# Kernel tuning notes

Hardware: AMD Instinct MI355X
Metric: run time of the kernel (lower is better)

The kernel has to match this reference:

```python
import jax, jax.numpy as jnp
import numpy as np
from jax import lax

DIM = 256
HEADS = 8
HIDDEN = int(DIM * 2.66)  # 680
KS = 3


def conv1x1(x, w, b):
    # x: (B,C,H,W), w: (O,C), b: (O,)
    return jnp.einsum('oc,bchw->bohw', w, x) + b[None, :, None, None]


def dwconv(x, w, b):
    # depthwise 3x3, SAME padding; w: (C,1,3,3)
    y = lax.conv_general_dilated(
        x, w, window_strides=(1, 1), padding='SAME',
        feature_group_count=x.shape[1],
        dimension_numbers=('NCHW', 'OIHW', 'NCHW'))
    return y + b[None, :, None, None]


def layernorm_c(x, w, b, eps=1e-5):
    # torch nn.LayerNorm(dim) applied on NHWC -> normalize over channel dim
    mu = jnp.mean(x, axis=1, keepdims=True)
    var = jnp.mean(jnp.square(x - mu), axis=1, keepdims=True)
    xn = (x - mu) * lax.rsqrt(var + eps)
    return xn * w[None, :, None, None] + b[None, :, None, None]


def l2norm(x, eps=1e-12):
    # F.normalize(dim=-1)
    n = jnp.sqrt(jnp.sum(jnp.square(x), axis=-1, keepdims=True))
    return x / jnp.maximum(n, eps)


def setup_inputs() -> dict:
    key = jax.random.key(0)
    ks = jax.random.split(key, 20)
    s = 0.02
    d = {
        'x': jax.random.normal(ks[0], (4, DIM, 128, 128), jnp.float32),
        'n1_w': jnp.ones((DIM,), jnp.float32),
        'n1_b': jnp.zeros((DIM,), jnp.float32),
        'temp': jnp.ones((HEADS, 1, 1), jnp.float32),
        'qkv_w': jax.random.normal(ks[1], (3 * DIM, DIM), jnp.float32) * s,
        'qkv_b': jnp.zeros((3 * DIM,), jnp.float32),
        'qkv_dw_w': jax.random.normal(ks[2], (3 * DIM, 1, KS, KS), jnp.float32) * s,
        'qkv_dw_b': jnp.zeros((3 * DIM,), jnp.float32),
        'attn_po_w': jax.random.normal(ks[3], (DIM, DIM), jnp.float32) * s,
        'attn_po_b': jnp.zeros((DIM,), jnp.float32),
        'n2_w': jnp.ones((DIM,), jnp.float32),
        'n2_b': jnp.zeros((DIM,), jnp.float32),
        'pin_w': jax.random.normal(ks[4], (2 * HIDDEN, DIM), jnp.float32) * s,
        'pin_b': jnp.zeros((2 * HIDDEN,), jnp.float32),
        'dw_w': jax.random.normal(ks[5], (2 * HIDDEN, 1, KS, KS), jnp.float32) * s,
        'dw_b': jnp.zeros((2 * HIDDEN,), jnp.float32),
        'pout_w': jax.random.normal(ks[6], (DIM, HIDDEN), jnp.float32) * s,
        'pout_b': jnp.zeros((DIM,), jnp.float32),
    }
    return d


def attention(x, temp, qkv_w, qkv_b, qkv_dw_w, qkv_dw_b, po_w, po_b):
    B, C, H, W = x.shape
    qkv = dwconv(conv1x1(x, qkv_w, qkv_b), qkv_dw_w, qkv_dw_b)  # (B,3C,H,W)
    q, k, v = jnp.split(qkv, 3, axis=1)
    hd = C // HEADS
    q = l2norm(q.reshape(B, HEADS, hd, H * W))
    k = l2norm(k.reshape(B, HEADS, hd, H * W))
    v = v.reshape(B, HEADS, hd, H * W)
    attn = jnp.einsum('bhcn,bhdn->bhcd', q, k) * temp  # (B,h,hd,hd) channel attn
    attn = jax.nn.softmax(attn, axis=-1)
    out = jnp.einsum('bhcd,bhdn->bhcn', attn, v).reshape(B, C, H, W)
    return conv1x1(out, po_w, po_b)


def ffn(x, pin_w, pin_b, dw_w, dw_b, pout_w, pout_b):
    y = dwconv(conv1x1(x, pin_w, pin_b), dw_w, dw_b)
    y1, y2 = jnp.split(y, 2, axis=1)
    y = y1 * jax.nn.gelu(y2, approximate=False)
    return conv1x1(y, pout_w, pout_b)


def reference(x, n1_w, n1_b, temp, qkv_w, qkv_b, qkv_dw_w, qkv_dw_b,
              attn_po_w, attn_po_b, n2_w, n2_b, pin_w, pin_b, dw_w, dw_b,
              pout_w, pout_b):
    x = x + attention(layernorm_c(x, n1_w, n1_b), temp, qkv_w, qkv_b,
                      qkv_dw_w, qkv_dw_b, attn_po_w, attn_po_b)
    x = x + ffn(layernorm_c(x, n2_w, n2_b), pin_w, pin_b, dw_w, dw_b,
                pout_w, pout_b)
    return x
```

## Files before the change

### kernel.cpp

```cpp
#include <hip/hip_runtime.h>
#include <hip/hip_bf16.h>

#define NPIX 16384
#define BATCH 4
#define DIM 256
#define HEADS 8
#define HD 32
#define CHQKV 768
#define HID 680
#define HID2 1360

typedef __attribute__((ext_vector_type(8))) short short8v;
typedef __attribute__((ext_vector_type(4))) float float4v;

__device__ __forceinline__ ushort bf_hi(float v) {
    unsigned u = __float_as_uint(v);
    u += 0x7fffu + ((u >> 16) & 1u);
    return (ushort)(u >> 16);
}
__device__ __forceinline__ float bf_tof(ushort h) {
    return __uint_as_float(((unsigned)h) << 16);
}
__device__ __forceinline__ void bf_split(float v, ushort &h, ushort &l) {
    h = bf_hi(v);
    l = bf_hi(v - bf_tof(h));
}

__global__ void zero_kernel(float* __restrict__ p, int n) {
    int i = blockIdx.x * blockDim.x + threadIdx.x;
    if (i < n) p[i] = 0.f;
}

__global__ void convert_weights(const float* __restrict__ qkv_w, const float* __restrict__ po_w,
                                const float* __restrict__ pin_w, const float* __restrict__ pout_w,
                                ushort* __restrict__ qH, ushort* __restrict__ qL,
                                ushort* __restrict__ oH, ushort* __restrict__ oL,
                                ushort* __restrict__ iH, ushort* __restrict__ iL,
                                ushort* __restrict__ uH, ushort* __restrict__ uL) {
    int i = blockIdx.x * 256 + threadIdx.x;
    const float* s; ushort *dh, *dl; int off;
    if (i < 196608)      { s = qkv_w;  dh = qH; dl = qL; off = i; }
    else if (i < 262144) { s = po_w;   dh = oH; dl = oL; off = i - 196608; }
    else if (i < 610304) { s = pin_w;  dh = iH; dl = iL; off = i - 262144; }
    else if (i < 784384) { s = pout_w; dh = uH; dl = uL; off = i - 610304; }
    else return;
    ushort h, l; bf_split(s[off], h, l);
    dh[off] = h; dl[off] = l;
}

__global__ void ln_fused(const float* __restrict__ x, const float* __restrict__ lw,
                         const float* __restrict__ lb, uint* __restrict__ XH,
                         uint* __restrict__ XL) {
    __shared__ float Ss[256], Ss2[256], muS[64], rsS[64], wS[256], bS[256];
    int t = threadIdx.x, px = t & 63, cg = t >> 6, c0 = cg * 64;
    int p = blockIdx.x * 64 + px;
    wS[t] = lw[t]; bS[t] = lb[t];
    float v[64]; float s = 0.f, s2 = 0.f;
    #pragma unroll
    for (int j = 0; j < 64; ++j) {
        v[j] = x[(size_t)(c0 + j) * NPIX + p];
        s += v[j]; s2 += v[j] * v[j];
    }
    Ss[t] = s; Ss2[t] = s2;
    __syncthreads();
    if (t < 64) {
        float ts = Ss[t] + Ss[t + 64] + Ss[t + 128] + Ss[t + 192];
        float t2 = Ss2[t] + Ss2[t + 64] + Ss2[t + 128] + Ss2[t + 192];
        float m = ts * (1.0f / DIM);
        float var = t2 * (1.0f / DIM) - m * m;
        muS[t] = m; rsS[t] = rsqrtf(var + 1e-5f);
    }
    __syncthreads();
    float m = muS[px], r = rsS[px];
    #pragma unroll
    for (int j = 0; j < 64; j += 2) {
        float a = (v[j] - m) * r * wS[c0 + j] + bS[c0 + j];
        float b2 = (v[j + 1] - m) * r * wS[c0 + j + 1] + bS[c0 + j + 1];
        ushort h0, l0, h1, l1; bf_split(a, h0, l0); bf_split(b2, h1, l1);
        size_t w = (size_t)((c0 + j) >> 1) * NPIX + p;
        XH[w] = (uint)h0 | ((uint)h1 << 16);
        XL[w] = (uint)l0 | ((uint)l1 << 16);
    }
}

template <bool RES>
__global__ void gemm_mfma(const ushort* __restrict__ WH, const ushort* __restrict__ WL,
                          const uint* __restrict__ BpH, const uint* __restrict__ BpL,
                          const float* __restrict__ bias, const float* __restrict__ res,
                          float* __restrict__ Out, int M, int K, int ksteps) {
    __shared__ uint BhL[128 * 20];
    __shared__ uint BlL[128 * 20];
    __shared__ float biasS[128];
    const int N = NPIX;
    int tid = threadIdx.x;
    int m0 = blockIdx.y * 128;
    int n0 = blockIdx.x * 128;
    int l = tid & 63;
    int wid = tid >> 6;
    int wr = wid >> 1, wc = wid & 1;
    int lr = l & 15, lk = l >> 4;
    int kp = tid & 15;
    int nn8 = (tid >> 4) * 8;

    if (tid < 128) biasS[tid] = (m0 + tid < M) ? bias[m0 + tid] : 0.f;

    float4v acc[4][4];
    #pragma unroll
    for (int i = 0; i < 4; ++i)
        #pragma unroll
        for (int j = 0; j < 4; ++j) acc[i][j] = (float4v)0.f;

    const int Kh = K >> 1;
    for (int ks = 0; ks < ksteps; ++ks) {
        int k0 = ks * 32;
        int kpg = (k0 >> 1) + kp;
        bool kin = kpg < Kh;
        int kpc = kin ? kpg : (Kh - 1);
        const uint* ph = &BpH[(size_t)kpc * N + n0 + nn8];
        const uint* pl = &BpL[(size_t)kpc * N + n0 + nn8];
        uint4 h0 = *(const uint4*)ph;
        uint4 h1 = *(const uint4*)(ph + 4);
        uint4 g0 = *(const uint4*)pl;
        uint4 g1 = *(const uint4*)(pl + 4);
        if (!kin) {
            h0 = make_uint4(0, 0, 0, 0); h1 = h0; g0 = h0; g1 = h0;
        }
        __syncthreads();
        int r0 = nn8 * 20 + kp;
        BhL[r0      ] = h0.x; BhL[r0 + 20] = h0.y; BhL[r0 + 40] = h0.z; BhL[r0 + 60] = h0.w;
        BhL[r0 + 80 ] = h1.x; BhL[r0 +100] = h1.y; BhL[r0 +120] = h1.z; BhL[r0 +140] = h1.w;
        BlL[r0      ] = g0.x; BlL[r0 + 20] = g0.y; BlL[r0 + 40] = g0.z; BlL[r0 + 60] = g0.w;
        BlL[r0 + 80 ] = g1.x; BlL[r0 +100] = g1.y; BlL[r0 +120] = g1.z; BlL[r0 +140] = g1.w;
        __syncthreads();

        short8v ah[4], al[4], bh[4], bl[4];
        int kk = k0 + lk * 8;
        bool kok = (kk + 7) < K;
        int kc = kok ? kk : 0;
        #pragma unroll
        for (int mi = 0; mi < 4; ++mi) {
            int arow = m0 + wr * 64 + mi * 16 + lr;
            bool ok = (arow < M) && kok;
            int arc = arow < M ? arow : (M - 1);
            short8v th = *(const short8v*)&WH[(size_t)arc * K + kc];
            short8v tl = *(const short8v*)&WL[(size_t)arc * K + kc];
            short8v z = (short8v)0;
            ah[mi] = ok ? th : z;
            al[mi] = ok ? tl : z;
        }
        #pragma unroll
        for (int ni = 0; ni < 4; ++ni) {
            int brow = wc * 64 + ni * 16 + lr;
            bh[ni] = *(const short8v*)&BhL[brow * 20 + lk * 4];
            bl[ni] = *(const short8v*)&BlL[brow * 20 + lk * 4];
        }
        #pragma unroll
        for (int mi = 0; mi < 4; ++mi)
            #pragma unroll
            for (int ni = 0; ni < 4; ++ni) {
                acc[mi][ni] = __builtin_amdgcn_mfma_f32_16x16x32_bf16(ah[mi], bh[ni], acc[mi][ni], 0, 0, 0);
                acc[mi][ni] = __builtin_amdgcn_mfma_f32_16x16x32_bf16(ah[mi], bl[ni], acc[mi][ni], 0, 0, 0);
                acc[mi][ni] = __builtin_amdgcn_mfma_f32_16x16x32_bf16(al[mi], bh[ni], acc[mi][ni], 0, 0, 0);
            }
    }

    int lr4 = lk * 4;
    #pragma unroll
    for (int mi = 0; mi < 4; ++mi) {
        #pragma unroll
        for (int ni = 0; ni < 4; ++ni) {
            int rloc = wr * 64 + mi * 16 + lr4;
            int col = n0 + wc * 64 + ni * 16 + lr;
            #pragma unroll
            for (int r = 0; r < 4; ++r) {
                int row = m0 + rloc + r;
                if (row < M) {
                    float v = acc[mi][ni][r] + biasS[rloc + r];
                    size_t o = (size_t)row * N + col;
                    if (RES) v += res[o];
                    Out[o] = v;
                }
            }
        }
    }
}

__global__ void dwconv_sumsq(const float* __restrict__ in, const float* __restrict__ w9,
                             const float* __restrict__ bias, float* __restrict__ out,
                             float* __restrict__ ssq, float* __restrict__ ssk) {
    __shared__ float T[34][132];
    __shared__ float red[256];
    int bid = blockIdx.x;
    int ch = bid >> 2, rt = bid & 3;
    int g0 = rt * 32;
    int t = threadIdx.x;
    const float* src = in + (size_t)ch * NPIX;
    int c4 = (t & 31) * 4;
    for (int rr = t >> 5; rr < 34; rr += 8) {
        int grow = g0 - 1 + rr;
        float4 v = make_float4(0.f, 0.f, 0.f, 0.f);
        if (grow >= 0 && grow < 128) v = *(const float4*)&src[grow * 128 + c4];
        *(float4*)&T[rr][c4 + 1] = v;
    }
    if (t < 34) { T[t][0] = 0.f; T[t][129] = 0.f; }
    float wgt[9];
    #pragma unroll
    for (int i = 0; i < 9; ++i) wgt[i] = w9[ch * 9 + i];
    float bi = bias[ch];
    __syncthreads();
    int w = t & 127;
    int jb = (t >> 7) * 16;
    float a0 = T[jb][w], a1 = T[jb][w + 1], a2 = T[jb][w + 2];
    float b0 = T[jb + 1][w], b1 = T[jb + 1][w + 1], b2 = T[jb + 1][w + 2];
    float sq = 0.f;
    float* dst = out + (size_t)ch * NPIX + (g0 + jb) * 128 + w;
    #pragma unroll
    for (int i = 0; i < 16; ++i) {
        float c0 = T[jb + i + 2][w], c1 = T[jb + i + 2][w + 1], c2 = T[jb + i + 2][w + 2];
        float acc = bi + wgt[0] * a0 + wgt[1] * a1 + wgt[2] * a2
                       + wgt[3] * b0 + wgt[4] * b1 + wgt[5] * b2
                       + wgt[6] * c0 + wgt[7] * c1 + wgt[8] * c2;
        dst[i * 128] = acc;
        sq += acc * acc;
        a0 = b0; a1 = b1; a2 = b2; b0 = c0; b1 = c1; b2 = c2;
    }
    if (ch < 512) {
        red[t] = sq;
        __syncthreads();
        for (int st = 128; st > 0; st >>= 1) {
            if (t < st) red[t] += red[t + st];
            __syncthreads();
        }
        if (t == 0) {
            float* d2 = (ch < DIM) ? &ssq[ch] : &ssk[ch - DIM];
            atomicAdd(d2, red[0]);
        }
    }
}

__global__ void gram_kernel(const float* __restrict__ qkv, float* __restrict__ G) {
    int hH = blockIdx.x;
    int n0 = blockIdx.y * 512;
    __shared__ float qs[32][68];
    __shared__ float ks[32][68];
    int tid = threadIdx.x;
    int c = tid >> 3;
    int lo = (tid & 7) * 8;
    int dbase = tid & 7;
    const float* qbase = qkv + ((size_t)hH * HD + c) * NPIX;
    const float* kbase = qbase + (size_t)DIM * NPIX;
    float acc[4] = {0.f, 0.f, 0.f, 0.f};
    for (int t0 = 0; t0 < 512; t0 += 64) {
        __syncthreads();
        *(float4*)&qs[c][lo]     = *(const float4*)&qbase[n0 + t0 + lo];
        *(float4*)&qs[c][lo + 4] = *(const float4*)&qbase[n0 + t0 + lo + 4];
        *(float4*)&ks[c][lo]     = *(const float4*)&kbase[n0 + t0 + lo];
        *(float4*)&ks[c][lo + 4] = *(const float4*)&kbase[n0 + t0 + lo + 4];
        __syncthreads();
        for (int t = 0; t < 64; ++t) {
            float qv = qs[c][t];
            #pragma unroll
            for (int j = 0; j < 4; ++j) acc[j] += qv * ks[dbase + 8 * j][t];
        }
    }
    float* Gb = G + hH * 1024 + c * 32;
    #pragma unroll
    for (int j = 0; j < 4; ++j) atomicAdd(&Gb[dbase + 8 * j], acc[j]);
}

__global__ void attn_softmax(const float* __restrict__ G, const float* __restrict__ ssq,
                             const float* __restrict__ ssk, const float* __restrict__ temp,
                             float* __restrict__ A) {
    int hH = blockIdx.x;
    int tid = threadIdx.x;
    int c = tid >> 5, d = tid & 31;
    float nq = fmaxf(sqrtf(ssq[hH * HD + c]), 1e-12f);
    float nk = fmaxf(sqrtf(ssk[hH * HD + d]), 1e-12f);
    float v = G[hH * 1024 + c * 32 + d] / (nq * nk) * temp[hH];
    float m = v;
    #pragma unroll
    for (int s = 1; s < 32; s <<= 1) m = fmaxf(m, __shfl_xor(m, s, 32));
    float e = expf(v - m);
    float ssum = e;
    #pragma unroll
    for (int s = 1; s < 32; s <<= 1) ssum += __shfl_xor(ssum, s, 32);
    A[hH * 1024 + c * 32 + d] = e / ssum;
}

__global__ void pv_kernel(const float* __restrict__ A, const float* __restrict__ qkv,
                          uint* __restrict__ VH, uint* __restrict__ VL) {
    int hH = blockIdx.x;
    int n = blockIdx.y * 256 + threadIdx.x;
    __shared__ float As[1024];
    for (int i = threadIdx.x; i < 1024; i += 256) As[i] = A[hH * 1024 + i];
    __syncthreads();
    const float* vbase = qkv + ((size_t)(512 + hH * HD)) * NPIX + n;
    float vv[32];
    #pragma unroll
    for (int d = 0; d < 32; ++d) vv[d] = vbase[(size_t)d * NPIX];
    #pragma unroll
    for (int cc = 0; cc < 32; cc += 2) {
        float a0 = 0.f, a1 = 0.f;
        #pragma unroll
        for (int d = 0; d < 32; ++d) {
            a0 += As[cc * 32 + d] * vv[d];
            a1 += As[cc * 32 + 32 + d] * vv[d];
        }
        ushort h0, l0, h1, l1; bf_split(a0, h0, l0); bf_split(a1, h1, l1);
        size_t w = (size_t)((hH * HD + cc) >> 1) * NPIX + n;
        VH[w] = (uint)h0 | ((uint)h1 << 16);
        VL[w] = (uint)l0 | ((uint)l1 << 16);
    }
}

__global__ void dwgate(const float* __restrict__ in, const float* __restrict__ w9,
                       const float* __restrict__ bias, uint* __restrict__ GH,
                       uint* __restrict__ GL) {
    __shared__ float T[4][18][132];
    int bid = blockIdx.x;
    int cp = bid >> 3, rt = bid & 7;
    int c0 = cp * 2;
    int g0 = rt * 16;
    int t = threadIdx.x;
    for (int idx = t; idx < 4 * 18 * 32; idx += 256) {
        int pl = idx / 576;
        int rem = idx - pl * 576;
        int rr = rem >> 5;
        int cc4 = (rem & 31) * 4;
        int ch = c0 + (pl & 1) + (pl >> 1) * HID;
        int grow = g0 - 1 + rr;
        float4 v = make_float4(0.f, 0.f, 0.f, 0.f);
        if (grow >= 0 && grow < 128)
            v = *(const float4*)&in[(size_t)ch * NPIX + grow * 128 + cc4];
        *(float4*)&T[pl][rr][cc4 + 1] = v;
    }
    if (t < 72) {
        int pl = t / 18, rr = t % 18;
        T[pl][rr][0] = 0.f; T[pl][rr][129] = 0.f;
    }
    float wg[4][9]; float bs[4];
    #pragma unroll
    for (int p = 0; p < 4; ++p) {
        int ch = c0 + (p & 1) + (p >> 1) * HID;
        bs[p] = bias[ch];
        #pragma unroll
        for (int i = 0; i < 9; ++i) wg[p][i] = w9[ch * 9 + i];
    }
    __syncthreads();
    int w = t & 127;
    int jb = (t >> 7) * 8;
    float A[4][3], B[4][3];
    #pragma unroll
    for (int p = 0; p < 4; ++p) {
        A[p][0] = T[p][jb][w];     A[p][1] = T[p][jb][w + 1];     A[p][2] = T[p][jb][w + 2];
        B[p][0] = T[p][jb + 1][w]; B[p][1] = T[p][jb + 1][w + 1]; B[p][2] = T[p][jb + 1][w + 2];
    }
    size_t wbase = (size_t)cp * NPIX + (g0 + jb) * 128 + w;
    #pragma unroll
    for (int i = 0; i < 8; ++i) {
        float o[4];
        #pragma unroll
        for (int p = 0; p < 4; ++p) {
            float cA = T[p][jb + i + 2][w], cB = T[p][jb + i + 2][w + 1], cC = T[p][jb + i + 2][w + 2];
            o[p] = bs[p] + wg[p][0] * A[p][0] + wg[p][1] * A[p][1] + wg[p][2] * A[p][2]
                         + wg[p][3] * B[p][0] + wg[p][4] * B[p][1] + wg[p][5] * B[p][2]
                         + wg[p][6] * cA + wg[p][7] * cB + wg[p][8] * cC;
            A[p][0] = B[p][0]; A[p][1] = B[p][1]; A[p][2] = B[p][2];
            B[p][0] = cA; B[p][1] = cB; B[p][2] = cC;
        }
        float g0f = 0.5f * o[2] * (1.0f + erff(o[2] * 0.70710678118654752f));
        float g1f = 0.5f * o[3] * (1.0f + erff(o[3] * 0.70710678118654752f));
        float r0 = o[0] * g0f, r1 = o[1] * g1f;
        ushort h0, l0, h1, l1; bf_split(r0, h0, l0); bf_split(r1, h1, l1);
        GH[wbase + i * 128] = (uint)h0 | ((uint)h1 << 16);
        GL[wbase + i * 128] = (uint)l0 | ((uint)l1 << 16);
    }
}

extern "C" void kernel_launch(void* const* d_in, const int* in_sizes, int n_in,
                              void* d_out, int out_size, void* d_ws, size_t ws_size,
                              hipStream_t stream) {
    const float* x        = (const float*)d_in[0];
    const float* n1w      = (const float*)d_in[1];
    const float* n1b      = (const float*)d_in[2];
    const float* temp     = (const float*)d_in[3];
    const float* qkv_w    = (const float*)d_in[4];
    const float* qkv_b    = (const float*)d_in[5];
    const float* qkv_dw_w = (const float*)d_in[6];
    const float* qkv_dw_b = (const float*)d_in[7];
    const float* po_w     = (const float*)d_in[8];
    const float* po_b     = (const float*)d_in[9];
    const float* n2w      = (const float*)d_in[10];
    const float* n2b      = (const float*)d_in[11];
    const float* pin_w    = (const float*)d_in[12];
    const float* pin_b    = (const float*)d_in[13];
    const float* dw_w     = (const float*)d_in[14];
    const float* dw_b     = (const float*)d_in[15];
    const float* pout_w   = (const float*)d_in[16];
    const float* pout_b   = (const float*)d_in[17];
    float* out = (float*)d_out;

    char* ws = (char*)d_ws;
    float* R0 = (float*)ws;
    char*  R1c = ws + 50331648;
    float* R1 = (float*)R1c;
    float* R2 = (float*)(ws + 100663296);
    char*  wb = ws + 189792256;
    ushort* WqkvH = (ushort*)wb;
    ushort* WqkvL = WqkvH + 196608;
    ushort* WpoH  = WqkvL + 196608;
    ushort* WpoL  = WpoH + 65536;
    ushort* WpinH = WpoL + 65536;
    ushort* WpinL = WpinH + 348160;
    ushort* WpoutH = WpinL + 348160;
    ushort* WpoutL = WpoutH + 174080;
    float* G     = (float*)(wb + 3137536);
    float* ssq   = G + 8192;
    float* ssk   = ssq + 256;
    float* attnA = ssk + 256;
    uint* XHp = (uint*)R1c;
    uint* XLp = XHp + 2097152;
    uint* VHp = (uint*)R1c;
    uint* VLp = XLp;
    uint* GHp = (uint*)R1c;
    uint* GLp = GHp + 5570560;

    convert_weights<<<3064, 256, 0, stream>>>(qkv_w, po_w, pin_w, pout_w,
                                              WqkvH, WqkvL, WpoH, WpoL,
                                              WpinH, WpinL, WpoutH, WpoutL);

    for (int b = 0; b < BATCH; ++b) {
        const float* xb = x + (size_t)b * DIM * NPIX;
        float* outb = out + (size_t)b * DIM * NPIX;

        ln_fused<<<256, 256, 0, stream>>>(xb, n1w, n1b, XHp, XLp);
        gemm_mfma<false><<<dim3(128, 6), 256, 0, stream>>>(
            WqkvH, WqkvL, XHp, XLp, qkv_b, nullptr, R0, CHQKV, DIM, 8);
        zero_kernel<<<34, 256, 0, stream>>>(G, 8704);
        dwconv_sumsq<<<CHQKV * 4, 256, 0, stream>>>(R0, qkv_dw_w, qkv_dw_b, R1, ssq, ssk);
        gram_kernel<<<dim3(8, 32), 256, 0, stream>>>(R1, G);
        attn_softmax<<<8, 1024, 0, stream>>>(G, ssq, ssk, temp, attnA);
        pv_kernel<<<dim3(8, 64), 256, 0, stream>>>(attnA, R1, VHp, VLp);
        gemm_mfma<true><<<dim3(128, 2), 256, 0, stream>>>(
            WpoH, WpoL, VHp, VLp, po_b, xb, outb, DIM, DIM, 8);

        ln_fused<<<256, 256, 0, stream>>>(outb, n2w, n2b, XHp, XLp);
        gemm_mfma<false><<<dim3(128, 11), 256, 0, stream>>>(
            WpinH, WpinL, XHp, XLp, pin_b, nullptr, R2, HID2, DIM, 8);
        dwgate<<<340 * 8, 256, 0, stream>>>(R2, dw_w, dw_b, GHp, GLp);
        gemm_mfma<true><<<dim3(128, 2), 256, 0, stream>>>(
            WpoutH, WpoutL, GHp, GLp, pout_b, outb, outb, DIM, HID, 22);
    }
}
```

Before: 1.550 ms.

## Double-buffer GEMM B tiles in LDS and use narrower N tiles for small-M GEMMs

Templates the bf16x3 MFMA GEMM on N-tile width and adds a double-buffered LDS pipeline. The next k-step's B tile is loaded from global memory into registers while the current tile is computed, which removes one barrier per iteration. The two M=256 GEMMs now use 64-wide N tiles so they launch twice as many blocks and fill more CUs. The cost is twice the LDS footprint and some extra registers for the prefetched data.

```diff
diff --git a/kernel.cpp b/kernel.cpp
--- a/kernel.cpp
+++ b/kernel.cpp
@@ -83,58 +83,85 @@
     }
 }
 
-template <bool RES>
+template <int NT, bool RES>
 __global__ void gemm_mfma(const ushort* __restrict__ WH, const ushort* __restrict__ WL,
                           const uint* __restrict__ BpH, const uint* __restrict__ BpL,
                           const float* __restrict__ bias, const float* __restrict__ res,
                           float* __restrict__ Out, int M, int K, int ksteps) {
-    __shared__ uint BhL[128 * 20];
-    __shared__ uint BlL[128 * 20];
+    constexpr int NI = NT / 32;
+    constexpr int CPT = NT / 16;
+    constexpr int NU = CPT / 4;
+    constexpr int LDSW = NT * 20;
+    __shared__ uint BhL[2][LDSW];
+    __shared__ uint BlL[2][LDSW];
     __shared__ float biasS[128];
     const int N = NPIX;
     int tid = threadIdx.x;
     int m0 = blockIdx.y * 128;
-    int n0 = blockIdx.x * 128;
+    int n0 = blockIdx.x * NT;
     int l = tid & 63;
     int wid = tid >> 6;
     int wr = wid >> 1, wc = wid & 1;
     int lr = l & 15, lk = l >> 4;
     int kp = tid & 15;
-    int nn8 = (tid >> 4) * 8;
+    int cb = (tid >> 4) * CPT;
 
     if (tid < 128) biasS[tid] = (m0 + tid < M) ? bias[m0 + tid] : 0.f;
 
-    float4v acc[4][4];
+    float4v acc[4][NI];
     #pragma unroll
     for (int i = 0; i < 4; ++i)
         #pragma unroll
-        for (int j = 0; j < 4; ++j) acc[i][j] = (float4v)0.f;
+        for (int j = 0; j < NI; ++j) acc[i][j] = (float4v)0.f;
 
     const int Kh = K >> 1;
-    for (int ks = 0; ks < ksteps; ++ks) {
-        int k0 = ks * 32;
-        int kpg = (k0 >> 1) + kp;
+    uint4 sh[NU], sl[NU];
+
+    auto LOADB = [&](int ks) {
+        int kpg = ks * 16 + kp;
         bool kin = kpg < Kh;
         int kpc = kin ? kpg : (Kh - 1);
-        const uint* ph = &BpH[(size_t)kpc * N + n0 + nn8];
-        const uint* pl = &BpL[(size_t)kpc * N + n0 + nn8];
-        uint4 h0 = *(const uint4*)ph;
-        uint4 h1 = *(const uint4*)(ph + 4);
-        uint4 g0 = *(const uint4*)pl;
-        uint4 g1 = *(const uint4*)(pl + 4);
+        const uint* ph = &BpH[(size_t)kpc * N + n0 + cb];
+        const uint* pl = &BpL[(size_t)kpc * N + n0 + cb];
+        #pragma unroll
+        for (int u = 0; u < NU; ++u) {
+            sh[u] = *(const uint4*)(ph + 4 * u);
+            sl[u] = *(const uint4*)(pl + 4 * u);
+        }
         if (!kin) {
-            h0 = make_uint4(0, 0, 0, 0); h1 = h0; g0 = h0; g1 = h0;
-        }
-        __syncthreads();
-        int r0 = nn8 * 20 + kp;
-        BhL[r0      ] = h0.x; BhL[r0 + 20] = h0.y; BhL[r0 + 40] = h0.z; BhL[r0 + 60] = h0.w;
-        BhL[r0 + 80 ] = h1.x; BhL[r0 +100] = h1.y; BhL[r0 +120] = h1.z; BhL[r0 +140] = h1.w;
-        BlL[r0      ] = g0.x; BlL[r0 + 20] = g0.y; BlL[r0 + 40] = g0.z; BlL[r0 + 60] = g0.w;
-        BlL[r0 + 80 ] = g1.x; BlL[r0 +100] = g1.y; BlL[r0 +120] = g1.z; BlL[r0 +140] = g1.w;
-        __syncthreads();
-
-        short8v ah[4], al[4], bh[4], bl[4];
-        int kk = k0 + lk * 8;
+            #pragma unroll
+            for (int u = 0; u < NU; ++u) {
+                sh[u] = make_uint4(0, 0, 0, 0);
+                sl[u] = make_uint4(0, 0, 0, 0);
+            }
+        }
+    };
+    auto STOREB = [&](int buf) {
+        #pragma unroll
+        for (int u = 0; u < NU; ++u) {
+            int base = (cb + 4 * u) * 20 + kp;
+            BhL[buf][base     ] = sh[u].x;
+            BhL[buf][base + 20] = sh[u].y;
+            BhL[buf][base + 40] = sh[u].z;
+            BhL[buf][base + 60] = sh[u].w;
+            BlL[buf][base     ] = sl[u].x;
+            BlL[buf][base + 20] = sl[u].y;
+            BlL[buf][base + 40] = sl[u].z;
+            BlL[buf][base + 60] = sl[u].w;
+        }
+    };
+
+    LOADB(0);
+    STOREB(0);
+    __syncthreads();
+    int cur = 0;
+
+    for (int ks = 0; ks < ksteps; ++ks) {
+        bool more = (ks + 1) < ksteps;
+        if (more) LOADB(ks + 1);
+
+        short8v ah[4], al[4];
+        int kk = ks * 32 + lk * 8;
         bool kok = (kk + 7) < K;
         int kc = kok ? kk : 0;
         #pragma unroll
@@ -148,29 +175,35 @@
             ah[mi] = ok ? th : z;
             al[mi] = ok ? tl : z;
         }
-        #pragma unroll
-        for (int ni = 0; ni < 4; ++ni) {
-            int brow = wc * 64 + ni * 16 + lr;
-            bh[ni] = *(const short8v*)&BhL[brow * 20 + lk * 4];
-            bl[ni] = *(const short8v*)&BlL[brow * 20 + lk * 4];
+        short8v bh[NI], bl[NI];
+        #pragma unroll
+        for (int ni = 0; ni < NI; ++ni) {
+            int brow = wc * (NI * 16) + ni * 16 + lr;
+            bh[ni] = *(const short8v*)&BhL[cur][brow * 20 + lk * 4];
+            bl[ni] = *(const short8v*)&BlL[cur][brow * 20 + lk * 4];
         }
         #pragma unroll
         for (int mi = 0; mi < 4; ++mi)
             #pragma unroll
-            for (int ni = 0; ni < 4; ++ni) {
+            for (int ni = 0; ni < NI; ++ni) {
                 acc[mi][ni] = __builtin_amdgcn_mfma_f32_16x16x32_bf16(ah[mi], bh[ni], acc[mi][ni], 0, 0, 0);
                 acc[mi][ni] = __builtin_amdgcn_mfma_f32_16x16x32_bf16(ah[mi], bl[ni], acc[mi][ni], 0, 0, 0);
                 acc[mi][ni] = __builtin_amdgcn_mfma_f32_16x16x32_bf16(al[mi], bh[ni], acc[mi][ni], 0, 0, 0);
             }
+        if (more) {
+            STOREB(cur ^ 1);
+            __syncthreads();
+            cur ^= 1;
+        }
     }
 
     int lr4 = lk * 4;
     #pragma unroll
     for (int mi = 0; mi < 4; ++mi) {
         #pragma unroll
-        for (int ni = 0; ni < 4; ++ni) {
+        for (int ni = 0; ni < NI; ++ni) {
             int rloc = wr * 64 + mi * 16 + lr4;
-            int col = n0 + wc * 64 + ni * 16 + lr;
+            int col = n0 + wc * (NI * 16) + ni * 16 + lr;
             #pragma unroll
             for (int r = 0; r < 4; ++r) {
                 int row = m0 + rloc + r;
@@ -434,21 +467,21 @@
         float* outb = out + (size_t)b * DIM * NPIX;
 
         ln_fused<<<256, 256, 0, stream>>>(xb, n1w, n1b, XHp, XLp);
-        gemm_mfma<false><<<dim3(128, 6), 256, 0, stream>>>(
+        gemm_mfma<128, false><<<dim3(128, 6), 256, 0, stream>>>(
             WqkvH, WqkvL, XHp, XLp, qkv_b, nullptr, R0, CHQKV, DIM, 8);
         zero_kernel<<<34, 256, 0, stream>>>(G, 8704);
         dwconv_sumsq<<<CHQKV * 4, 256, 0, stream>>>(R0, qkv_dw_w, qkv_dw_b, R1, ssq, ssk);
         gram_kernel<<<dim3(8, 32), 256, 0, stream>>>(R1, G);
         attn_softmax<<<8, 1024, 0, stream>>>(G, ssq, ssk, temp, attnA);
         pv_kernel<<<dim3(8, 64), 256, 0, stream>>>(attnA, R1, VHp, VLp);
-        gemm_mfma<true><<<dim3(128, 2), 256, 0, stream>>>(
+        gemm_mfma<64, true><<<dim3(256, 2), 256, 0, stream>>>(
             WpoH, WpoL, VHp, VLp, po_b, xb, outb, DIM, DIM, 8);
 
         ln_fused<<<256, 256, 0, stream>>>(outb, n2w, n2b, XHp, XLp);
-        gemm_mfma<false><<<dim3(128, 11), 256, 0, stream>>>(
+        gemm_mfma<128, false><<<dim3(128, 11), 256, 0, stream>>>(
             WpinH, WpinL, XHp, XLp, pin_b, nullptr, R2, HID2, DIM, 8);
         dwgate<<<340 * 8, 256, 0, stream>>>(R2, dw_w, dw_b, GHp, GLp);
-        gemm_mfma<true><<<dim3(128, 2), 256, 0, stream>>>(
+        gemm_mfma<64, true><<<dim3(256, 2), 256, 0, stream>>>(
             WpoutH, WpoutL, GHp, GLp, pout_b, outb, outb, DIM, HID, 22);
     }
 }
```

After: 1.569 ms. No clear change (+1.2%).
